# Optimization experiments

Hardware: AMD Instinct MI355X
Metric: run time of the kernel (lower is better)

The kernel has to match this reference:

```python
import jax, jax.numpy as jnp
import numpy as np

DEG = [1, 72, 201, 816, 1790, 3756, 6923, 12768, 20286, 31710, 51623, 82296, 124280, 177576, 251115, 326064, 395760, 456840, 506179, 516200, 507003, 493746, 489256, 453936, 420025, 411320, 427761, 420700, 420500, 426780, 414284, 407008, 394053, 360910, 322245, 313704, 282902, 270940, 237783, 209000, 193766, 177870, 162110, 144848, 121230, 112700, 93483, 88512, 72275, 80700, 68799, 56784, 42665, 30996, 25630, 12936, 9804, 8584, 5251, 3480, 3111, 2728, 1890, 1472, 1235, 330, 201, 68, 69, 0, 71]
_d = np.array(DEG, dtype=np.float64)
AVG_LOG = float((np.log(np.arange(len(_d)) + 1.0) * _d).sum() / _d.sum())  # avg_deg['log']

N_NODES, N_EDGES, N_GRAPHS = 10000, 100000, 64
TOWERS, F, F_OUT, N_LAYERS = 5, 75, 15, 4


def setup_inputs() -> dict:
    key = jax.random.key(0)
    ks = jax.random.split(key, 32)
    r = lambda i, shape: jax.random.normal(ks[i], shape, jnp.float32) * 0.1
    return {
        "x": jax.random.normal(ks[0], (N_NODES, 14), jnp.float32),
        "edge_index": jax.random.randint(ks[1], (2, N_EDGES), 0, N_NODES, dtype=jnp.int32),
        "edge_attr": jax.random.normal(ks[2], (N_EDGES, 4), jnp.float32),
        "batch": jnp.sort(jax.random.randint(ks[3], (N_NODES,), 0, N_GRAPHS, dtype=jnp.int32)),
        "node_emb_w": r(4, (14, F)), "node_emb_b": r(5, (F,)),
        "edge_emb_w": r(6, (4, 50)), "edge_emb_b": r(7, (50,)),
        "ee_w": r(8, (N_LAYERS, 50, F)), "ee_b": r(9, (N_LAYERS, F)),
        "pre_w": r(10, (N_LAYERS, TOWERS, 3 * F, F)), "pre_b": r(11, (N_LAYERS, TOWERS, F)),
        "post_w": r(12, (N_LAYERS, TOWERS, 13 * F, F_OUT)), "post_b": r(13, (N_LAYERS, TOWERS, F_OUT)),
        "lin_w": r(14, (N_LAYERS, F, F)), "lin_b": r(15, (N_LAYERS, F)),
        "bn_g": jnp.ones((N_LAYERS, F), jnp.float32), "bn_b": jnp.zeros((N_LAYERS, F), jnp.float32),
        "mlp_w1": r(16, (F, 50)), "mlp_b1": r(17, (50,)),
        "mlp_w2": r(18, (50, 25)), "mlp_b2": r(19, (25,)),
        "mlp_w3": r(20, (25, 1)), "mlp_b3": r(21, (1,)),
    }


def _pna_conv(x, src, dst, ea, ee_w, ee_b, pre_w, pre_b, post_w, post_b, lin_w, lin_b):
    # x: [N, F]; ea: [E, edge_dim]; divide_input=False so every tower sees full F.
    N = x.shape[0]
    e = ea @ ee_w + ee_b                                   # edge_encoder  [E, F]
    h = jnp.concatenate([x[dst], x[src], e], axis=-1)       # [x_i, x_j, e] [E, 3F]
    m = jnp.einsum('ef,tfg->etg', h, pre_w) + pre_b         # per-tower pre nn [E, T, F]
    cnt = jax.ops.segment_sum(jnp.ones((m.shape[0],), x.dtype), dst, N)  # in-degree [N]
    cnt1 = jnp.maximum(cnt, 1.0)[:, None, None]
    mean = jax.ops.segment_sum(m, dst, N) / cnt1
    mean_sq = jax.ops.segment_sum(m * m, dst, N) / cnt1
    std = jnp.sqrt(jax.nn.relu(mean_sq - mean * mean) + 1e-5)
    has = (cnt > 0)[:, None, None]
    mn = jnp.where(has, jax.ops.segment_min(m, dst, N), 0.0)
    mx = jnp.where(has, jax.ops.segment_max(m, dst, N), 0.0)
    agg = jnp.concatenate([mean, mn, mx, std], axis=-1)     # [N, T, 4F]
    scl = jnp.log(cnt1 + 1.0) / AVG_LOG                     # amplification scaler
    out = jnp.concatenate([agg, agg * scl, agg / scl], -1)  # identity/amp/atten [N, T, 12F]
    x_rep = jnp.broadcast_to(x[:, None, :], (N, TOWERS, x.shape[1]))
    out = jnp.concatenate([x_rep, out], axis=-1)            # [N, T, 13F]
    out = jnp.einsum('ntf,tfg->ntg', out, post_w) + post_b  # per-tower post nn [N, T, F_out]
    return out.reshape(N, -1) @ lin_w + lin_b               # [N, F]


def _bn(x, g, b):
    mu = x.mean(0)
    var = x.var(0)  # biased, as torch BatchNorm1d uses for normalization
    return (x - mu) * jax.lax.rsqrt(var + 1e-5) * g + b


def reference(x, edge_index, edge_attr, batch, node_emb_w, node_emb_b, edge_emb_w, edge_emb_b,
              ee_w, ee_b, pre_w, pre_b, post_w, post_b, lin_w, lin_b, bn_g, bn_b,
              mlp_w1, mlp_b1, mlp_w2, mlp_b2, mlp_w3, mlp_b3):
    src, dst = edge_index[0], edge_index[1]
    h = x @ node_emb_w + node_emb_b
    ea = edge_attr @ edge_emb_w + edge_emb_b
    for i in range(N_LAYERS):
        h = jax.nn.relu(_bn(_pna_conv(h, src, dst, ea, ee_w[i], ee_b[i], pre_w[i], pre_b[i],
                                      post_w[i], post_b[i], lin_w[i], lin_b[i]), bn_g[i], bn_b[i]))
    per_atom = h
    g = jax.ops.segment_sum(h, batch, N_GRAPHS)             # global_add_pool [G, F]
    g = jax.nn.relu(g @ mlp_w1 + mlp_b1)
    g = jax.nn.relu(g @ mlp_w2 + mlp_b2)
    g = (g @ mlp_w3 + mlp_b3).reshape(-1)                   # num_out==1 -> view(-1)
    return (g, per_atom)
```

## Files before the change

kernel.cpp:

```cpp
#include <hip/hip_runtime.h>
#include <math.h>

#define NN 10000
#define NE 100000
#define NGR 64
#define NT 5
#define FD 75
#define FOUT 15
#define NLAY 4
#define MAXB 1792

typedef __bf16 bf16;
typedef __bf16 bf16x8 __attribute__((ext_vector_type(8)));
typedef float f32x4 __attribute__((ext_vector_type(4)));

__device__ inline unsigned pk2(float a, float b) {
  bf16 x = (bf16)a, y = (bf16)b;
  unsigned short ux, uy;
  __builtin_memcpy(&ux, &x, 2); __builtin_memcpy(&uy, &y, 2);
  return (unsigned)ux | ((unsigned)uy << 16);
}


__global__ __launch_bounds__(256) void k_node_emb(const float* __restrict__ x,
    const float* __restrict__ w, const float* __restrict__ b, bf16* __restrict__ hbf) {
  int idx = blockIdx.x * 256 + threadIdx.x;
  if (idx >= NN * FD) return;
  int n = idx / FD, f = idx - n * FD;
  float acc = b[f];
#pragma unroll
  for (int k = 0; k < 14; ++k) acc += x[n * 14 + k] * w[k * FD + f];
  hbf[n * 80 + f] = (bf16)acc;
}

__global__ __launch_bounds__(256) void k_edge_emb(const float* __restrict__ eattr,
    const float* __restrict__ w, const float* __restrict__ b, bf16* __restrict__ eabf) {
  int idx = blockIdx.x * 256 + threadIdx.x;
  if (idx >= NE * 50) return;
  int e = idx / 50, c = idx - e * 50;
  float acc = b[c];
#pragma unroll
  for (int k = 0; k < 4; ++k) acc += eattr[e * 4 + k] * w[k * 50 + c];
  eabf[e * 56 + c] = (bf16)acc;
}

__global__ __launch_bounds__(256) void k_count(const int* __restrict__ dst, int* __restrict__ deg) {
  int e = blockIdx.x * 256 + threadIdx.x;
  if (e < NE) atomicAdd(&deg[dst[e]], 1);
}

__global__ __launch_bounds__(1024) void k_scan(const int* __restrict__ deg, int* __restrict__ rowptr) {
  __shared__ int buf[1024];
  __shared__ int carry;
  int tid = threadIdx.x;
  if (tid == 0) carry = 0;
  __syncthreads();
  for (int base = 0; base < NN; base += 1024) {
    int i = base + tid;
    int v = (i < NN) ? deg[i] : 0;
    buf[tid] = v;
    __syncthreads();
    for (int off = 1; off < 1024; off <<= 1) {
      int t = (tid >= off) ? buf[tid - off] : 0;
      __syncthreads();
      buf[tid] += t;
      __syncthreads();
    }
    int inc = buf[tid];
    int tot = buf[1023];
    if (i < NN) rowptr[i + 1] = carry + inc;
    __syncthreads();
    if (tid == 0) carry += tot;
    __syncthreads();
  }
  if (tid == 0) rowptr[0] = 0;
}

__global__ __launch_bounds__(256) void k_scl(const int* __restrict__ deg, float* __restrict__ scl,
                                             float* __restrict__ iscl, float inv_avg_log) {
  int n = blockIdx.x * 256 + threadIdx.x;
  if (n >= NN) return;
  float c1 = fmaxf((float)deg[n], 1.f);
  float s = logf(c1 + 1.f) * inv_avg_log;
  scl[n] = s;
  iscl[n] = 1.f / s;
}

__global__ __launch_bounds__(256) void k_scatter(const int* __restrict__ dst, const int* __restrict__ rowptr,
    int* __restrict__ cursor, int* __restrict__ eids) {
  int e = blockIdx.x * 256 + threadIdx.x;
  if (e >= NE) return;
  int d = dst[e];
  int pos = rowptr[d] + atomicAdd(&cursor[d], 1);
  eids[pos] = e;
}

__global__ __launch_bounds__(256) void k_next(const int* __restrict__ rowptr, int* __restrict__ nxt) {
  int n = blockIdx.x * 256 + threadIdx.x;
  if (n >= NN) return;
  int base = rowptr[n];
  int lo = n + 1, hi = min(n + 128, NN);
  while (lo < hi) {
    int mid = (lo + hi + 1) >> 1;
    if (rowptr[mid] - base <= 128) lo = mid; else hi = mid - 1;
  }
  nxt[n] = lo;
}

__global__ __launch_bounds__(1024) void k_walk(const int* __restrict__ nxt,
    int* __restrict__ bstart, int* __restrict__ nblk) {
  __shared__ int lnx[NN];
  int tid = threadIdx.x;
  for (int i = tid; i < NN; i += 1024) lnx[i] = nxt[i];
  __syncthreads();
  if (tid == 0) {
    int b = 0, n = 0;
    while (n < NN && b < MAXB) { bstart[b++] = n; n = lnx[n]; }
    bstart[b] = NN;
    nblk[0] = b;
  }
}


__global__ __launch_bounds__(256) void k_combine(const float* __restrict__ pre_wA,
    const float* __restrict__ pre_bA, const float* __restrict__ ee_wA, const float* __restrict__ ee_bA,
    bf16* __restrict__ WctA, float* __restrict__ bcA) {
  const int l = blockIdx.y;
  const float* pre_w = pre_wA + (size_t)l * NT * 225 * FD;
  const float* pre_b = pre_bA + (size_t)l * NT * FD;
  const float* ee_w  = ee_wA + (size_t)l * 50 * FD;
  const float* ee_b  = ee_bA + (size_t)l * FD;
  bf16* Wct = WctA + (size_t)l * 384 * 256;
  float* bc = bcA + (size_t)l * 384;
  int idx = blockIdx.x * 256 + threadIdx.x;
  if (idx >= 384 * 256) return;
  int c = idx >> 8, s = idx & 255;
  int t = c / 75, g = c - t * 75;
  int chunk = s >> 6, within = s & 63, sblk = within >> 3, elem = within & 7;
  int lb = sblk ^ (c & 7);
  int k = chunk * 64 + lb * 8 + elem;
  float v = 0.f;
  if (c < 375) {
    if (k < 75)                    v = pre_w[(t * 225 + k) * 75 + g];
    else if (k >= 80 && k < 155)   v = pre_w[(t * 225 + 75 + (k - 80)) * 75 + g];
    else if (k >= 160 && k < 210) {
      int kk = k - 160;
      float a = 0.f;
      for (int f2 = 0; f2 < 75; ++f2) a += ee_w[kk * 75 + f2] * pre_w[(t * 225 + 150 + f2) * 75 + g];
      v = a;
    }
  }
  Wct[c * 256 + s] = (bf16)v;
  if (s == 0) {
    float a = 0.f;
    if (c < 375) {
      a = pre_b[t * 75 + g];
      for (int f2 = 0; f2 < 75; ++f2) a += ee_b[f2] * pre_w[(t * 225 + 150 + f2) * 75 + g];
    }
    bc[c] = a;
  }
}

__global__ __launch_bounds__(256) void k_PL(const float* __restrict__ pwA,
    const float* __restrict__ lwA, float* __restrict__ PLA) {
  const int l = blockIdx.y;
  const float* pw = pwA + (size_t)l * NT * 975 * FOUT;
  const float* lw = lwA + (size_t)l * FD * FD;
  float* PL = PLA + (size_t)l * 5 * 975 * 80;
  int idx = blockIdx.x * 256 + threadIdx.x;
  if (idx >= 5 * 975 * 80) return;
  int t = idx / (975 * 80), rem = idx - t * 975 * 80;
  int row = rem / 80, o = rem - row * 80;
  float v = 0.f;
  if (o < 75) {
#pragma unroll
    for (int j = 0; j < 15; ++j)
      v += pw[((size_t)t * 975 + row) * 15 + j] * lw[(t * 15 + j) * 75 + o];
  }
  PL[idx] = v;
}

__global__ __launch_bounds__(256) void k_combine2b(const float* __restrict__ PLA,
    bf16* __restrict__ Wct2A) {
  const int l = blockIdx.y;
  const float* PL = PLA + (size_t)l * 5 * 975 * 80;
  bf16* Wct2 = Wct2A + (size_t)l * 256 * 1664;
  int idx = blockIdx.x * 256 + threadIdx.x;
  if (idx >= 256 * 1664) return;
  int c = idx / 1664, s = idx - c * 1664;
  int chunk = s >> 6, within = s & 63, sblk = within >> 3, elem = within & 7;
  int lb = sblk ^ (c & 7);
  int k = chunk * 64 + lb * 8 + elem;
  int g2 = c / 80, o = c - g2 * 80;
  float val = 0.f;
  if (c < 240 && o < 75) {
    if (k < 75) {
      if (g2 == 0) {
#pragma unroll
        for (int t = 0; t < 5; ++t) val += PL[(t * 975 + k) * 80 + o];
      }
    } else if (k >= 80 && k < 1616) {
      int q = k - 80;
      int si = q / 384, cc = q - si * 384;
      if (cc < 375) {
        int t = cc / 75, g = cc - t * 75;
        int row = 75 + g2 * 300 + si * 75 + g;
        val = PL[((size_t)t * 975 + row) * 80 + o];
      }
    }
  }
  Wct2[(size_t)c * 1664 + s] = (bf16)val;
}

__global__ __launch_bounds__(128) void k_zbias(const float* __restrict__ pbA,
    const float* __restrict__ lwA, const float* __restrict__ lbA, float* __restrict__ zbA) {
  const int l = blockIdx.y;
  const float* pb = pbA + (size_t)l * NT * FOUT;
  const float* lw = lwA + (size_t)l * FD * FD;
  const float* lb = lbA + (size_t)l * FD;
  float* zb = zbA + (size_t)l * 80;
  int o = threadIdx.x;
  if (o >= 80) return;
  float val = 0.f;
  if (o < 75) {
    val = lb[o];
    for (int t = 0; t < 5; ++t)
      for (int j = 0; j < 15; ++j)
        val += pb[t * 15 + j] * lw[(t * 15 + j) * 75 + o];
  }
  zb[o] = val;
}


#define APTR_(g_, pd_, ps_, pe_) \
  ((g_) < 10 ? (pd_) + (g_) * 8 : (g_) < 20 ? (ps_) + ((g_) - 10) * 8 : \
   (g_) < 27 ? (pe_) + ((g_) - 20) * 8 : zerobuf)

#define LOADA(c_) do { int g_ = (c_) * 8 + slb;                \
    pa0 = *(const uint4*)APTR_(g_, pd0, ps0, pe0);             \
    pa1 = *(const uint4*)APTR_(g_, pd1, ps1, pe1);             \
    pa2 = *(const uint4*)APTR_(g_, pd2, ps2, pe2);             \
    pa3 = *(const uint4*)APTR_(g_, pd3, ps3, pe3); } while (0)

#define LOADB(ntb_, c_) do {                                                      \
    const bf16* wp_ = Wct + (size_t)((ntb_) + sr) * 256 + (c_) * 64 + slb * 8;    \
    pq0 = *(const uint4*)(wp_ + 0 * 8192);                                        \
    pq1 = *(const uint4*)(wp_ + 1 * 8192);                                        \
    pq2 = *(const uint4*)(wp_ + 2 * 8192);                                        \
    pq3 = *(const uint4*)(wp_ + 3 * 8192); } while (0)

#define STORE_AB() do { int swz_ = (slb ^ (sr & 7)) << 4;       \
    *(uint4*)(As + (0 * 32 + sr) * 128 + swz_) = pa0;           \
    *(uint4*)(As + (1 * 32 + sr) * 128 + swz_) = pa1;           \
    *(uint4*)(As + (2 * 32 + sr) * 128 + swz_) = pa2;           \
    *(uint4*)(As + (3 * 32 + sr) * 128 + swz_) = pa3;           \
    *(uint4*)(Bs + (0 * 32 + sr) * 128 + (slb << 4)) = pq0;     \
    *(uint4*)(Bs + (1 * 32 + sr) * 128 + (slb << 4)) = pq1;     \
    *(uint4*)(Bs + (2 * 32 + sr) * 128 + (slb << 4)) = pq2;     \
    *(uint4*)(Bs + (3 * 32 + sr) * 128 + (slb << 4)) = pq3; } while (0)

__global__ __launch_bounds__(256) void k_pre_fused(
    const bf16* __restrict__ hbf, const bf16* __restrict__ eabf,
    const int* __restrict__ eids, const int* __restrict__ srcA, const int* __restrict__ dstA,
    const int* __restrict__ rowptr, const int* __restrict__ bstart, const int* __restrict__ nblk,
    const bf16* __restrict__ Wct, const float* __restrict__ bc,
    const bf16* __restrict__ zerobuf, bf16* __restrict__ aggbf2) {
  __shared__ __align__(16) unsigned char smem[33792];
  unsigned char* As = smem;
  unsigned char* Bs = smem + 16384;
  bf16* m_lds = (bf16*)smem;
  __shared__ const bf16* pDl[128];
  __shared__ const bf16* pSl[128];
  __shared__ const bf16* pEl[128];
  __shared__ int nodeRows[129];
  __shared__ int nq[5];

  const int b = blockIdx.x;
  if (b >= nblk[0]) return;
  const int ntb = blockIdx.y * 128;
  const int tid = threadIdx.x;
  const int n0b = bstart[b], n1b = bstart[b + 1];
  const int rbase = rowptr[n0b];
  const int nrows = rowptr[n1b] - rbase;
  const int nnod = n1b - n0b;

  if (tid == 0) { nq[0] = 0; nq[1] = 0; nq[2] = 0; nq[3] = 0; nq[4] = nnod; }
  if (tid < 128) {
    if (tid < nrows) {
      int e = eids[rbase + tid];
      pDl[tid] = hbf + dstA[e] * 80;
      pSl[tid] = hbf + srcA[e] * 80;
      pEl[tid] = eabf + e * 56;
    } else { pDl[tid] = zerobuf; pSl[tid] = zerobuf; pEl[tid] = zerobuf; }
  }
  if (tid <= nnod) nodeRows[tid] = rowptr[n0b + tid] - rbase;
  __syncthreads();
  if (tid < nnod) {
#pragma unroll
    for (int q = 1; q <= 3; ++q) {
      int target = (nrows * q) >> 2;
      if (nodeRows[tid] < target && nodeRows[tid + 1] >= target) nq[q] = tid + 1;
    }
  }

  const int lane = tid & 63;
  const int wave = tid >> 6;
  const int wr = wave >> 1, wc = wave & 1;
  const int l15 = lane & 15, l4 = lane >> 4;
  const int sr = tid >> 3, slb = tid & 7;

  const bf16 *pd0 = pDl[sr],      *ps0 = pSl[sr],      *pe0 = pEl[sr];
  const bf16 *pd1 = pDl[32 + sr], *ps1 = pSl[32 + sr], *pe1 = pEl[32 + sr];
  const bf16 *pd2 = pDl[64 + sr], *ps2 = pSl[64 + sr], *pe2 = pEl[64 + sr];
  const bf16 *pd3 = pDl[96 + sr], *ps3 = pSl[96 + sr], *pe3 = pEl[96 + sr];

  f32x4 acc[4][4];
  f32x4 zv = {0.f, 0.f, 0.f, 0.f};
#pragma unroll
  for (int i = 0; i < 4; ++i)
#pragma unroll
    for (int j = 0; j < 4; ++j) acc[i][j] = zv;

  uint4 pa0, pa1, pa2, pa3, pq0, pq1, pq2, pq3;
  LOADA(0); LOADB(ntb, 0);

#pragma unroll
  for (int c = 0; c < 4; ++c) {
    STORE_AB();
    __syncthreads();
    if (c < 3) { LOADA(c + 1); LOADB(ntb, c + 1); }
#pragma unroll
    for (int kk = 0; kk < 2; ++kk) {
      int kb = kk * 4 + l4;
      bf16x8 af[4], bfv[4];
#pragma unroll
      for (int i = 0; i < 4; ++i) {
        int row = wr * 64 + i * 16 + l15;
        af[i] = *(const bf16x8*)(As + row * 128 + ((kb ^ (row & 7)) << 4));
      }
#pragma unroll
      for (int j = 0; j < 4; ++j) {
        int col = wc * 64 + j * 16 + l15;
        bfv[j] = *(const bf16x8*)(Bs + col * 128 + ((kb ^ (col & 7)) << 4));
      }
#pragma unroll
      for (int i = 0; i < 4; ++i)
#pragma unroll
        for (int j = 0; j < 4; ++j)
          acc[i][j] = __builtin_amdgcn_mfma_f32_16x16x32_bf16(af[i], bfv[j], acc[i][j], 0, 0, 0);
    }
    __syncthreads();
  }

  float bcv[4];
#pragma unroll
  for (int j = 0; j < 4; ++j) bcv[j] = bc[ntb + wc * 64 + j * 16 + l15];
#pragma unroll
  for (int i = 0; i < 4; ++i) {
    int R = wr * 64 + i * 16 + l4 * 4;
#pragma unroll
    for (int j = 0; j < 4; ++j) {
      int col = wc * 64 + j * 16 + l15;
#pragma unroll
      for (int q = 0; q < 4; ++q)
        m_lds[(R + q) * 132 + col] = (bf16)(acc[i][j][q] + bcv[j]);
    }
  }
  __syncthreads();

  {
    const int cp = tid & 63;
    const int qq = tid >> 6;
    const unsigned char* mb = (const unsigned char*)m_lds;
    for (int i = nq[qq]; i < nq[qq + 1]; ++i) {
      int ra = nodeRows[i], rb2 = nodeRows[i + 1];
      float s0 = 0.f, q0 = 0.f, a0 = INFINITY, b0 = -INFINITY;
      float s1 = 0.f, q1 = 0.f, a1 = INFINITY, b1 = -INFINITY;
      for (int r = ra; r < rb2; ++r) {
        unsigned u = *(const unsigned*)(mb + r * 264 + cp * 4);
        float v0 = __uint_as_float(u << 16);
        float v1 = __uint_as_float(u & 0xffff0000u);
        s0 += v0; q0 += v0 * v0; a0 = fminf(a0, v0); b0 = fmaxf(b0, v0);
        s1 += v1; q1 += v1 * v1; a1 = fminf(a1, v1); b1 = fmaxf(b1, v1);
      }
      int d = rb2 - ra;
      float inv = 1.f / ((d > 0) ? (float)d : 1.f);
      float m0 = s0 * inv, m1 = s1 * inv;
      float sd0 = sqrtf(fmaxf(q0 * inv - m0 * m0, 0.f) + 1e-5f);
      float sd1 = sqrtf(fmaxf(q1 * inv - m1 * m1, 0.f) + 1e-5f);
      if (d == 0) { a0 = 0.f; b0 = 0.f; a1 = 0.f; b1 = 0.f; }
      bf16* ag = aggbf2 + (size_t)(n0b + i) * 1536 + ntb + cp * 2;
      *(unsigned*)(ag)        = pk2(m0, m1);
      *(unsigned*)(ag + 384)  = pk2(a0, a1);
      *(unsigned*)(ag + 768)  = pk2(b0, b1);
      *(unsigned*)(ag + 1152) = pk2(sd0, sd1);
    }
  }
}


#define APG_(g_) ((nA >= NN || (g_) >= 202) ? zerobuf : \
    ((g_) < 10 ? hbf + nA * 80 + (g_) * 8 : aggbf2 + (size_t)nA * 1536 + ((g_) - 10) * 8))

#define LOADP4(c_) do {                                                 \
    int gA_ = (c_) * 16 + slb;                                          \
    pa0 = *(const uint4*)APG_(gA_);                                     \
    pa1 = *(const uint4*)APG_(gA_ + 8);                                 \
    int ko_ = (c_) * 128 + slb * 8;                                     \
    pb0 = *(const uint4*)(pc0 + ko_);                                   \
    pb1 = *(const uint4*)(pc0 + ko_ + 64);                              \
    pb2 = *(const uint4*)(pc1 + ko_);                                   \
    pb3 = *(const uint4*)(pc1 + ko_ + 64);                              \
    pb4 = *(const uint4*)(pc2 + ko_);                                   \
    pb5 = *(const uint4*)(pc2 + ko_ + 64);                              \
    pb6 = *(const uint4*)(pc3 + ko_);                                   \
    pb7 = *(const uint4*)(pc3 + ko_ + 64);                              \
  } while (0)

__global__ __launch_bounds__(256) void k_post4(const bf16* __restrict__ hbf,
    const bf16* __restrict__ aggbf2, const bf16* __restrict__ Wct2,
    const float* __restrict__ zb, const float* __restrict__ scl, const float* __restrict__ iscl,
    const bf16* __restrict__ zerobuf, float* __restrict__ z, float* __restrict__ stat_raw_l) {
  __shared__ __align__(16) unsigned char smem[40960];
  unsigned char* As = smem;
  unsigned char* Bs = smem + 8192;
  float* Ps = (float*)smem;
  __shared__ float sclS[32], isclS[32];
  const int n0 = blockIdx.x * 32;
  const int y  = blockIdx.y;
  const int tid = threadIdx.x;
  const int lane = tid & 63, wave = tid >> 6;
  const int l15 = lane & 15, l4 = lane >> 4;
  const int sr = tid >> 3, slb = tid & 7;
  const int nA = n0 + sr;

  const bf16 *pc0, *pc1, *pc2, *pc3;
  {
    int c0 = sr, c1 = sr + 32, c2 = sr + 64, c3 = sr + 96;
    int l0 = (c0 / 40) * 80 + y * 40 + (c0 % 40);
    int l1 = (c1 / 40) * 80 + y * 40 + (c1 % 40);
    int l2 = (c2 / 40) * 80 + y * 40 + (c2 % 40);
    int l3 = (c3 < 120) ? ((c3 / 40) * 80 + y * 40 + (c3 % 40)) : 0;
    pc0 = Wct2 + (size_t)l0 * 1664;
    pc1 = Wct2 + (size_t)l1 * 1664;
    pc2 = Wct2 + (size_t)l2 * 1664;
    pc3 = Wct2 + (size_t)l3 * 1664;
  }
  if (tid < 32) {
    int n = n0 + tid;
    sclS[tid] = (n < NN) ? scl[n] : 0.f;
    isclS[tid] = (n < NN) ? iscl[n] : 0.f;
  }

  f32x4 acc[2][2];
  f32x4 zvv = {0.f, 0.f, 0.f, 0.f};
#pragma unroll
  for (int i = 0; i < 2; ++i)
#pragma unroll
    for (int j = 0; j < 2; ++j) acc[i][j] = zvv;

  uint4 pa0, pa1, pb0, pb1, pb2, pb3, pb4, pb5, pb6, pb7;
  LOADP4(0);
  for (int c = 0; c < 13; ++c) {
    {
      int s1_ = (slb ^ (sr & 7)) << 4;
      *(uint4*)(As + sr * 256 + s1_) = pa0;
      *(uint4*)(As + sr * 256 + s1_ + 128) = pa1;
      *(uint4*)(Bs + (sr)      * 256 + (slb << 4)) = pb0;
      *(uint4*)(Bs + (sr)      * 256 + (slb << 4) + 128) = pb1;
      *(uint4*)(Bs + (sr + 32) * 256 + (slb << 4)) = pb2;
      *(uint4*)(Bs + (sr + 32) * 256 + (slb << 4) + 128) = pb3;
      *(uint4*)(Bs + (sr + 64) * 256 + (slb << 4)) = pb4;
      *(uint4*)(Bs + (sr + 64) * 256 + (slb << 4) + 128) = pb5;
      *(uint4*)(Bs + (sr + 96) * 256 + (slb << 4)) = pb6;
      *(uint4*)(Bs + (sr + 96) * 256 + (slb << 4) + 128) = pb7;
    }
    __syncthreads();
    if (c < 12) LOADP4(c + 1);
#pragma unroll
    for (int kk = 0; kk < 4; ++kk) {
      int kb = kk * 4 + l4;
      bf16x8 af[2], bv[2];
#pragma unroll
      for (int i = 0; i < 2; ++i) {
        int row = i * 16 + l15;
        af[i] = *(const bf16x8*)(As + row * 256 + (((kb & 8) | ((kb & 7) ^ (row & 7))) << 4));
      }
#pragma unroll
      for (int j = 0; j < 2; ++j) {
        int cidx = wave * 32 + j * 16 + l15;
        bv[j] = *(const bf16x8*)(Bs + cidx * 256 + (((kb & 8) | ((kb & 7) ^ (cidx & 7))) << 4));
      }
#pragma unroll
      for (int i = 0; i < 2; ++i)
#pragma unroll
        for (int j = 0; j < 2; ++j)
          acc[i][j] = __builtin_amdgcn_mfma_f32_16x16x32_bf16(af[i], bv[j], acc[i][j], 0, 0, 0);
    }
    __syncthreads();
  }

#pragma unroll
  for (int i = 0; i < 2; ++i) {
#pragma unroll
    for (int j = 0; j < 2; ++j) {
      int cidx = wave * 32 + j * 16 + l15;
#pragma unroll
      for (int q = 0; q < 4; ++q)
        Ps[(i * 16 + l4 * 4 + q) * 132 + cidx] = acc[i][j][q];
    }
  }
  __syncthreads();

  float v0_, v1_, v2_, v3_, v4_;
  int r0_, r1_, r2_, r3_, r4_, f0_, f1_, f2_, f3_, f4_;
#define EPI(t_, vv_, rr_, ff_) do {                                           \
    int idx_ = tid + (t_) * 256;                                              \
    rr_ = idx_ / 40; ff_ = idx_ - rr_ * 40;                                   \
    int n_ = n0 + rr_, zc_ = y * 40 + ff_;                                    \
    float v_ = 0.f;                                                           \
    if (n_ < NN && zc_ < 75) {                                                \
      v_ = Ps[rr_ * 132 + ff_] + sclS[rr_] * Ps[rr_ * 132 + 40 + ff_]         \
         + isclS[rr_] * Ps[rr_ * 132 + 80 + ff_] + zb[zc_];                   \
      z[n_ * 75 + zc_] = v_;                                                  \
    }                                                                         \
    vv_ = v_;                                                                 \
  } while (0)
  EPI(0, v0_, r0_, f0_); EPI(1, v1_, r1_, f1_); EPI(2, v2_, r2_, f2_);
  EPI(3, v3_, r3_, f3_); EPI(4, v4_, r4_, f4_);
#undef EPI
  __syncthreads();
  Ps[r0_ * 132 + f0_] = v0_;
  Ps[r1_ * 132 + f1_] = v1_;
  Ps[r2_ * 132 + f2_] = v2_;
  Ps[r3_ * 132 + f3_] = v3_;
  Ps[r4_ * 132 + f4_] = v4_;
  __syncthreads();
  if (tid < 40) {
    int zc = y * 40 + tid;
    if (zc < 75) {
      float s = 0.f, s2 = 0.f;
#pragma unroll
      for (int r = 0; r < 32; ++r) {
        float v = Ps[r * 132 + tid];
        s += v; s2 += v * v;
      }
      atomicAdd(&stat_raw_l[zc], s);
      atomicAdd(&stat_raw_l[75 + zc], s2);
    }
  }
}

__global__ __launch_bounds__(256) void k_bnapply(const float* __restrict__ z,
    const float* __restrict__ stat_raw, const float* __restrict__ g, const float* __restrict__ b,
    float* __restrict__ outF, bf16* __restrict__ hbf) {
  int idx = blockIdx.x * 256 + threadIdx.x;
  if (idx >= NN * FD) return;
  int n = idx / FD, f = idx - n * FD;
  float mu = stat_raw[f] * (1.f / NN);
  float var = stat_raw[75 + f] * (1.f / NN) - mu * mu;
  var = fmaxf(var, 0.f);
  float rs = 1.f / sqrtf(var + 1e-5f);
  float v = (z[idx] - mu) * rs * g[f] + b[f];
  v = fmaxf(v, 0.f);
  if (outF) outF[idx] = v;
  hbf[n * 80 + f] = (bf16)v;
}

__global__ __launch_bounds__(256) void k_pool(const float* __restrict__ h, const int* __restrict__ batch,
                                              float* __restrict__ gpool) {
  int idx = blockIdx.x * 256 + threadIdx.x;
  if (idx >= NN * FD) return;
  int n = idx / FD, f = idx - n * FD;
  atomicAdd(&gpool[batch[n] * FD + f], h[idx]);
}

__global__ __launch_bounds__(256) void k_mlp(const float* __restrict__ gpool,
    const float* __restrict__ w1, const float* __restrict__ b1,
    const float* __restrict__ w2, const float* __restrict__ b2,
    const float* __restrict__ w3, const float* __restrict__ b3,
    float* __restrict__ out) {
  __shared__ float G[NGR * FD];
  __shared__ float G1[NGR * 50];
  __shared__ float G2[NGR * 25];
  int tid = threadIdx.x;
  for (int i = tid; i < NGR * FD; i += 256) G[i] = gpool[i];
  __syncthreads();
  for (int i = tid; i < NGR * 50; i += 256) {
    int r = i / 50, c = i - r * 50;
    float a = b1[c];
    for (int k = 0; k < FD; ++k) a += G[r * FD + k] * w1[k * 50 + c];
    G1[i] = fmaxf(a, 0.f);
  }
  __syncthreads();
  for (int i = tid; i < NGR * 25; i += 256) {
    int r = i / 25, c = i - r * 25;
    float a = b2[c];
    for (int k = 0; k < 50; ++k) a += G1[r * 50 + k] * w2[k * 25 + c];
    G2[i] = fmaxf(a, 0.f);
  }
  __syncthreads();
  if (tid < NGR) {
    float a = b3[0];
    for (int k = 0; k < 25; ++k) a += G2[tid * 25 + k] * w3[k];
    out[tid] = a;
  }
}


extern "C" void kernel_launch(void* const* d_in, const int* in_sizes, int n_in,
                              void* d_out, int out_size, void* d_ws, size_t ws_size,
                              hipStream_t stream) {
  (void)in_sizes; (void)n_in; (void)out_size; (void)ws_size;
  const float* x      = (const float*)d_in[0];
  const int*   eidx   = (const int*)  d_in[1];
  const float* eattr  = (const float*)d_in[2];
  const int*   batch  = (const int*)  d_in[3];
  const float* nw     = (const float*)d_in[4];
  const float* nb     = (const float*)d_in[5];
  const float* ew     = (const float*)d_in[6];
  const float* ebias  = (const float*)d_in[7];
  const float* ee_w   = (const float*)d_in[8];
  const float* ee_b   = (const float*)d_in[9];
  const float* pre_w  = (const float*)d_in[10];
  const float* pre_b  = (const float*)d_in[11];
  const float* post_w = (const float*)d_in[12];
  const float* post_b = (const float*)d_in[13];
  const float* lin_w  = (const float*)d_in[14];
  const float* lin_b  = (const float*)d_in[15];
  const float* bn_g   = (const float*)d_in[16];
  const float* bn_b   = (const float*)d_in[17];
  const float* w1 = (const float*)d_in[18];
  const float* b1 = (const float*)d_in[19];
  const float* w2 = (const float*)d_in[20];
  const float* b2 = (const float*)d_in[21];
  const float* w3 = (const float*)d_in[22];
  const float* b3 = (const float*)d_in[23];

  const int* srcA = eidx;
  const int* dstA = eidx + NE;

  char* base = (char*)d_ws;
  size_t off = 0;
  auto alloc = [&](size_t bytes) -> char* {
    char* p = base + off;
    off = (off + bytes + 255) & ~(size_t)255;
    return p;
  };
  bf16*  hbf    = (bf16*) alloc((size_t)NN * 80 * 2);
  bf16*  eabf   = (bf16*) alloc((size_t)NE * 56 * 2);
  bf16*  aggbf2 = (bf16*) alloc((size_t)NN * 1536 * 2);
  float* z      = (float*)alloc((size_t)NN * FD * 4);
  bf16*  WctA   = (bf16*) alloc((size_t)NLAY * 384 * 256 * 2);
  float* bcA    = (float*)alloc((size_t)NLAY * 384 * 4);
  bf16*  Wct2A  = (bf16*) alloc((size_t)NLAY * 256 * 1664 * 2);
  float* zbA    = (float*)alloc((size_t)NLAY * 80 * 4);
  float* PLA    = (float*)alloc((size_t)NLAY * 5 * 975 * 80 * 4);
  float* scl    = (float*)alloc(NN * 4);
  float* iscl   = (float*)alloc(NN * 4);
  int*   deg    = (int*)alloc(NN * 4);
  int*   rowptr = (int*)alloc((NN + 1) * 4);
  int*   cursor = (int*)alloc(NN * 4);
  int*   eids   = (int*)alloc(NE * 4);
  int*   nxt    = (int*)alloc(NN * 4);
  int*   bstart = (int*)alloc((MAXB + 1) * 4);
  int*   nblk   = (int*)alloc(16);
  float* stat_all = (float*)alloc((size_t)NLAY * 160 * 4);
  float* gpool  = (float*)alloc(NGR * FD * 4);
  bf16*  zerobuf = (bf16*)alloc(256);

  static const int DEG_TAB[71] = {1, 72, 201, 816, 1790, 3756, 6923, 12768, 20286, 31710,
    51623, 82296, 124280, 177576, 251115, 326064, 395760, 456840, 506179, 516200, 507003,
    493746, 489256, 453936, 420025, 411320, 427761, 420700, 420500, 426780, 414284, 407008,
    394053, 360910, 322245, 313704, 282902, 270940, 237783, 209000, 193766, 177870, 162110,
    144848, 121230, 112700, 93483, 88512, 72275, 80700, 68799, 56784, 42665, 30996, 25630,
    12936, 9804, 8584, 5251, 3480, 3111, 2728, 1890, 1472, 1235, 330, 201, 68, 69, 0, 71};
  double num = 0.0, den = 0.0;
  for (int i = 0; i < 71; ++i) { num += log((double)i + 1.0) * DEG_TAB[i]; den += DEG_TAB[i]; }
  float inv_avg_log = (float)(den / num);

  hipMemsetAsync(deg, 0, NN * 4, stream);
  hipMemsetAsync(cursor, 0, NN * 4, stream);
  hipMemsetAsync(gpool, 0, NGR * FD * 4, stream);
  hipMemsetAsync(stat_all, 0, (size_t)NLAY * 160 * 4, stream);
  hipMemsetAsync(zerobuf, 0, 256, stream);

  k_node_emb<<<(NN * FD + 255) / 256, 256, 0, stream>>>(x, nw, nb, hbf);
  k_edge_emb<<<(NE * 50 + 255) / 256, 256, 0, stream>>>(eattr, ew, ebias, eabf);
  k_count<<<(NE + 255) / 256, 256, 0, stream>>>(dstA, deg);
  k_scan<<<1, 1024, 0, stream>>>(deg, rowptr);
  k_scl<<<(NN + 255) / 256, 256, 0, stream>>>(deg, scl, iscl, inv_avg_log);
  k_scatter<<<(NE + 255) / 256, 256, 0, stream>>>(dstA, rowptr, cursor, eids);
  k_next<<<(NN + 255) / 256, 256, 0, stream>>>(rowptr, nxt);
  k_walk<<<1, 1024, 0, stream>>>(nxt, bstart, nblk);

  {
    dim3 gc(384, NLAY);
    k_combine<<<gc, 256, 0, stream>>>(pre_w, pre_b, ee_w, ee_b, WctA, bcA);
    dim3 gp((5 * 975 * 80 + 255) / 256, NLAY);
    k_PL<<<gp, 256, 0, stream>>>(post_w, lin_w, PLA);
    dim3 g2((256 * 1664 + 255) / 256, NLAY);
    k_combine2b<<<g2, 256, 0, stream>>>(PLA, Wct2A);
    dim3 gz(1, NLAY);
    k_zbias<<<gz, 128, 0, stream>>>(post_b, lin_w, lin_b, zbA);
  }

  float* outp = (float*)d_out;
  for (int l = 0; l < NLAY; ++l) {
    dim3 gpref(MAXB, 3);
    k_pre_fused<<<gpref, 256, 0, stream>>>(hbf, eabf, eids, srcA, dstA, rowptr, bstart, nblk,
        WctA + (size_t)l * 384 * 256, bcA + (size_t)l * 384, zerobuf, aggbf2);
    dim3 gpost((NN + 31) / 32, 2);
    k_post4<<<gpost, 256, 0, stream>>>(hbf, aggbf2, Wct2A + (size_t)l * 256 * 1664,
        zbA + (size_t)l * 80, scl, iscl, zerobuf, z, stat_all + (size_t)l * 160);
    float* wdst = (l == NLAY - 1) ? (outp + NGR) : nullptr;
    k_bnapply<<<(NN * FD + 255) / 256, 256, 0, stream>>>(z, stat_all + (size_t)l * 160,
        bn_g + (size_t)l * FD, bn_b + (size_t)l * FD, wdst, hbf);
  }

  k_pool<<<(NN * FD + 255) / 256, 256, 0, stream>>>(outp + NGR, batch, gpool);
  k_mlp<<<1, 256, 0, stream>>>(gpool, w1, b1, w2, b2, w3, b3, outp);
}
```

Baseline: 564.6 us.

## Fold edge embedding into pre-tower weights to shrink GEMM K from 256 to 192

Composes the edge-embedding weight with each layer's edge-encoder weight on device (W12), then folds that into the pre-tower weights, so the pre GEMM consumes the raw 4-dim edge attributes, padded to 8 bf16, instead of a 50-dim edge embedding. This cuts the K dimension of the pre GEMM from four 64-wide chunks to three and shrinks the per-edge gather from 56 to 8 bf16. Edge-embedding materialisation is replaced by a trivial pad kernel. The cost is one extra tiny precompute kernel and slightly different rounding, since bf16 inputs now multiply composed weights.

```diff
diff --git a/kernel.cpp b/kernel.cpp
--- a/kernel.cpp
+++ b/kernel.cpp
@@ -33,15 +33,12 @@
   hbf[n * 80 + f] = (bf16)acc;
 }
 
-__global__ __launch_bounds__(256) void k_edge_emb(const float* __restrict__ eattr,
-    const float* __restrict__ w, const float* __restrict__ b, bf16* __restrict__ eabf) {
+__global__ __launch_bounds__(256) void k_edge4(const float* __restrict__ eattr,
+    bf16* __restrict__ eabf4) {
   int idx = blockIdx.x * 256 + threadIdx.x;
-  if (idx >= NE * 50) return;
-  int e = idx / 50, c = idx - e * 50;
-  float acc = b[c];
-#pragma unroll
-  for (int k = 0; k < 4; ++k) acc += eattr[e * 4 + k] * w[k * 50 + c];
-  eabf[e * 56 + c] = (bf16)acc;
+  if (idx >= NE * 8) return;
+  int e = idx >> 3, c = idx & 7;
+  eabf4[idx] = (c < 4) ? (bf16)eattr[e * 4 + c] : (bf16)0.f;
 }
 
 __global__ __launch_bounds__(256) void k_count(const int* __restrict__ dst, int* __restrict__ deg) {
@@ -122,19 +119,40 @@
 }
 
 
+__global__ __launch_bounds__(256) void k_W12(const float* __restrict__ ew,
+    const float* __restrict__ ebias, const float* __restrict__ ee_wA, const float* __restrict__ ee_bA,
+    float* __restrict__ W12A, float* __restrict__ bcombA) {
+  const int l = blockIdx.y;
+  const float* ee_w = ee_wA + (size_t)l * 50 * FD;
+  const float* ee_b = ee_bA + (size_t)l * FD;
+  int idx = blockIdx.x * 256 + threadIdx.x;
+  if (idx >= 375) return;
+  if (idx < 300) {
+    int d = idx / 75, o = idx - d * 75;
+    float v = 0.f;
+    for (int j = 0; j < 50; ++j) v += ew[d * 50 + j] * ee_w[j * 75 + o];
+    W12A[(size_t)l * 300 + idx] = v;
+  } else {
+    int o = idx - 300;
+    float v = ee_b[o];
+    for (int j = 0; j < 50; ++j) v += ebias[j] * ee_w[j * 75 + o];
+    bcombA[(size_t)l * 80 + o] = v;
+  }
+}
+
 __global__ __launch_bounds__(256) void k_combine(const float* __restrict__ pre_wA,
-    const float* __restrict__ pre_bA, const float* __restrict__ ee_wA, const float* __restrict__ ee_bA,
+    const float* __restrict__ pre_bA, const float* __restrict__ W12A, const float* __restrict__ bcombA,
     bf16* __restrict__ WctA, float* __restrict__ bcA) {
   const int l = blockIdx.y;
   const float* pre_w = pre_wA + (size_t)l * NT * 225 * FD;
   const float* pre_b = pre_bA + (size_t)l * NT * FD;
-  const float* ee_w  = ee_wA + (size_t)l * 50 * FD;
-  const float* ee_b  = ee_bA + (size_t)l * FD;
-  bf16* Wct = WctA + (size_t)l * 384 * 256;
+  const float* W12   = W12A + (size_t)l * 300;
+  const float* bcomb = bcombA + (size_t)l * 80;
+  bf16* Wct = WctA + (size_t)l * 384 * 192;
   float* bc = bcA + (size_t)l * 384;
   int idx = blockIdx.x * 256 + threadIdx.x;
-  if (idx >= 384 * 256) return;
-  int c = idx >> 8, s = idx & 255;
+  if (idx >= 384 * 192) return;
+  int c = idx / 192, s = idx - c * 192;
   int t = c / 75, g = c - t * 75;
   int chunk = s >> 6, within = s & 63, sblk = within >> 3, elem = within & 7;
   int lb = sblk ^ (c & 7);
@@ -143,19 +161,19 @@
   if (c < 375) {
     if (k < 75)                    v = pre_w[(t * 225 + k) * 75 + g];
     else if (k >= 80 && k < 155)   v = pre_w[(t * 225 + 75 + (k - 80)) * 75 + g];
-    else if (k >= 160 && k < 210) {
-      int kk = k - 160;
+    else if (k >= 160 && k < 164) {
+      int d = k - 160;
       float a = 0.f;
-      for (int f2 = 0; f2 < 75; ++f2) a += ee_w[kk * 75 + f2] * pre_w[(t * 225 + 150 + f2) * 75 + g];
+      for (int f2 = 0; f2 < 75; ++f2) a += W12[d * 75 + f2] * pre_w[(t * 225 + 150 + f2) * 75 + g];
       v = a;
     }
   }
-  Wct[c * 256 + s] = (bf16)v;
+  Wct[c * 192 + s] = (bf16)v;
   if (s == 0) {
     float a = 0.f;
     if (c < 375) {
       a = pre_b[t * 75 + g];
-      for (int f2 = 0; f2 < 75; ++f2) a += ee_b[f2] * pre_w[(t * 225 + 150 + f2) * 75 + g];
+      for (int f2 = 0; f2 < 75; ++f2) a += bcomb[f2] * pre_w[(t * 225 + 150 + f2) * 75 + g];
     }
     bc[c] = a;
   }
@@ -234,7 +252,7 @@
 
 #define APTR_(g_, pd_, ps_, pe_) \
   ((g_) < 10 ? (pd_) + (g_) * 8 : (g_) < 20 ? (ps_) + ((g_) - 10) * 8 : \
-   (g_) < 27 ? (pe_) + ((g_) - 20) * 8 : zerobuf)
+   (g_) < 21 ? (pe_) : zerobuf)
 
 #define LOADA(c_) do { int g_ = (c_) * 8 + slb;                \
     pa0 = *(const uint4*)APTR_(g_, pd0, ps0, pe0);             \
@@ -243,11 +261,11 @@
     pa3 = *(const uint4*)APTR_(g_, pd3, ps3, pe3); } while (0)
 
 #define LOADB(ntb_, c_) do {                                                      \
-    const bf16* wp_ = Wct + (size_t)((ntb_) + sr) * 256 + (c_) * 64 + slb * 8;    \
-    pq0 = *(const uint4*)(wp_ + 0 * 8192);                                        \
-    pq1 = *(const uint4*)(wp_ + 1 * 8192);                                        \
-    pq2 = *(const uint4*)(wp_ + 2 * 8192);                                        \
-    pq3 = *(const uint4*)(wp_ + 3 * 8192); } while (0)
+    const bf16* wp_ = Wct + (size_t)((ntb_) + sr) * 192 + (c_) * 64 + slb * 8;    \
+    pq0 = *(const uint4*)(wp_ + 0 * 6144);                                        \
+    pq1 = *(const uint4*)(wp_ + 1 * 6144);                                        \
+    pq2 = *(const uint4*)(wp_ + 2 * 6144);                                        \
+    pq3 = *(const uint4*)(wp_ + 3 * 6144); } while (0)
 
 #define STORE_AB() do { int swz_ = (slb ^ (sr & 7)) << 4;       \
     *(uint4*)(As + (0 * 32 + sr) * 128 + swz_) = pa0;           \
@@ -260,7 +278,7 @@
     *(uint4*)(Bs + (3 * 32 + sr) * 128 + (slb << 4)) = pq3; } while (0)
 
 __global__ __launch_bounds__(256) void k_pre_fused(
-    const bf16* __restrict__ hbf, const bf16* __restrict__ eabf,
+    const bf16* __restrict__ hbf, const bf16* __restrict__ eabf4,
     const int* __restrict__ eids, const int* __restrict__ srcA, const int* __restrict__ dstA,
     const int* __restrict__ rowptr, const int* __restrict__ bstart, const int* __restrict__ nblk,
     const bf16* __restrict__ Wct, const float* __restrict__ bc,
@@ -290,7 +308,7 @@
       int e = eids[rbase + tid];
       pDl[tid] = hbf + dstA[e] * 80;
       pSl[tid] = hbf + srcA[e] * 80;
-      pEl[tid] = eabf + e * 56;
+      pEl[tid] = eabf4 + e * 8;
     } else { pDl[tid] = zerobuf; pSl[tid] = zerobuf; pEl[tid] = zerobuf; }
   }
   if (tid <= nnod) nodeRows[tid] = rowptr[n0b + tid] - rbase;
@@ -325,10 +343,10 @@
   LOADA(0); LOADB(ntb, 0);
 
 #pragma unroll
-  for (int c = 0; c < 4; ++c) {
+  for (int c = 0; c < 3; ++c) {
     STORE_AB();
     __syncthreads();
-    if (c < 3) { LOADA(c + 1); LOADB(ntb, c + 1); }
+    if (c < 2) { LOADA(c + 1); LOADB(ntb, c + 1); }
 #pragma unroll
     for (int kk = 0; kk < 2; ++kk) {
       int kb = kk * 4 + l4;
@@ -648,14 +666,16 @@
     return p;
   };
   bf16*  hbf    = (bf16*) alloc((size_t)NN * 80 * 2);
-  bf16*  eabf   = (bf16*) alloc((size_t)NE * 56 * 2);
+  bf16*  eabf4  = (bf16*) alloc((size_t)NE * 8 * 2);
   bf16*  aggbf2 = (bf16*) alloc((size_t)NN * 1536 * 2);
   float* z      = (float*)alloc((size_t)NN * FD * 4);
-  bf16*  WctA   = (bf16*) alloc((size_t)NLAY * 384 * 256 * 2);
+  bf16*  WctA   = (bf16*) alloc((size_t)NLAY * 384 * 192 * 2);
   float* bcA    = (float*)alloc((size_t)NLAY * 384 * 4);
   bf16*  Wct2A  = (bf16*) alloc((size_t)NLAY * 256 * 1664 * 2);
   float* zbA    = (float*)alloc((size_t)NLAY * 80 * 4);
   float* PLA    = (float*)alloc((size_t)NLAY * 5 * 975 * 80 * 4);
+  float* W12A   = (float*)alloc((size_t)NLAY * 300 * 4);
+  float* bcombA = (float*)alloc((size_t)NLAY * 80 * 4);
   float* scl    = (float*)alloc(NN * 4);
   float* iscl   = (float*)alloc(NN * 4);
   int*   deg    = (int*)alloc(NN * 4);
@@ -686,7 +706,7 @@
   hipMemsetAsync(zerobuf, 0, 256, stream);
 
   k_node_emb<<<(NN * FD + 255) / 256, 256, 0, stream>>>(x, nw, nb, hbf);
-  k_edge_emb<<<(NE * 50 + 255) / 256, 256, 0, stream>>>(eattr, ew, ebias, eabf);
+  k_edge4<<<(NE * 8 + 255) / 256, 256, 0, stream>>>(eattr, eabf4);
   k_count<<<(NE + 255) / 256, 256, 0, stream>>>(dstA, deg);
   k_scan<<<1, 1024, 0, stream>>>(deg, rowptr);
   k_scl<<<(NN + 255) / 256, 256, 0, stream>>>(deg, scl, iscl, inv_avg_log);
@@ -695,8 +715,10 @@
   k_walk<<<1, 1024, 0, stream>>>(nxt, bstart, nblk);
 
   {
-    dim3 gc(384, NLAY);
-    k_combine<<<gc, 256, 0, stream>>>(pre_w, pre_b, ee_w, ee_b, WctA, bcA);
+    dim3 gw(2, NLAY);
+    k_W12<<<gw, 256, 0, stream>>>(ew, ebias, ee_w, ee_b, W12A, bcombA);
+    dim3 gc((384 * 192 + 255) / 256, NLAY);
+    k_combine<<<gc, 256, 0, stream>>>(pre_w, pre_b, W12A, bcombA, WctA, bcA);
     dim3 gp((5 * 975 * 80 + 255) / 256, NLAY);
     k_PL<<<gp, 256, 0, stream>>>(post_w, lin_w, PLA);
     dim3 g2((256 * 1664 + 255) / 256, NLAY);
@@ -708,8 +730,8 @@
   float* outp = (float*)d_out;
   for (int l = 0; l < NLAY; ++l) {
     dim3 gpref(MAXB, 3);
-    k_pre_fused<<<gpref, 256, 0, stream>>>(hbf, eabf, eids, srcA, dstA, rowptr, bstart, nblk,
-        WctA + (size_t)l * 384 * 256, bcA + (size_t)l * 384, zerobuf, aggbf2);
+    k_pre_fused<<<gpref, 256, 0, stream>>>(hbf, eabf4, eids, srcA, dstA, rowptr, bstart, nblk,
+        WctA + (size_t)l * 384 * 192, bcA + (size_t)l * 384, zerobuf, aggbf2);
     dim3 gpost((NN + 31) / 32, 2);
     k_post4<<<gpost, 256, 0, stream>>>(hbf, aggbf2, Wct2A + (size_t)l * 256 * 1664,
         zbA + (size_t)l * 80, scl, iscl, zerobuf, z, stat_all + (size_t)l * 160);
```

Result: no change. 568.6 us (+0.7%).
